# Performance work log

Measured on AMD Instinct MI355X. Metric: run time of the kernel, lower is better.

## Reference

```python
import jax, jax.numpy as jnp
import numpy as np
import math

B = 524288
D = 4
CTX = 64
HID = 128
IN_DIM = 2 + CTX  # keep_idx len is 2 for every mask
# default_masks_D(4, 10) dedups to exactly these 4 masks (torch module therefore has 4 layers)
KEEP = ((0, 1), (1, 2), (2, 3), (0, 3))
TRANS = ((2, 3), (0, 3), (0, 1), (1, 2))
L = 4


def _mlp(x, W1, b1, W2, b2, W3, b3):
    # MLP(in_dim, out_dim, hidden=128, depth=2): Lin+GELU, Lin+GELU, Lin
    x = jax.nn.gelu(x @ W1 + b1, approximate=False)
    x = jax.nn.gelu(x @ W2 + b2, approximate=False)
    return x @ W3 + b3


def setup_inputs() -> dict:
    key = jax.random.key(0)
    ks = jax.random.split(key, 16)
    theta = jax.random.normal(ks[0], (B, D), dtype=jnp.float32)
    h = jax.random.normal(ks[1], (B, CTX), dtype=jnp.float32)
    p = lambda k, shape: jax.random.normal(k, shape, dtype=jnp.float32) * 0.02
    inp = {"theta": theta, "h": h}
    # stacked per-layer weights for s_net and t_net
    for pref, off in (("s", 2), ("t", 8)):
        inp[pref + "W1"] = p(ks[off + 0], (L, IN_DIM, HID))
        inp[pref + "b1"] = p(ks[off + 1], (L, HID))
        inp[pref + "W2"] = p(ks[off + 2], (L, HID, HID))
        inp[pref + "b2"] = p(ks[off + 3], (L, HID))
        inp[pref + "W3"] = p(ks[off + 4], (L, HID, 2))
        inp[pref + "b3"] = p(ks[off + 5], (L, 2))
    return inp


def reference(theta, h, sW1, sb1, sW2, sb2, sW3, sb3, tW1, tb1, tW2, tb2, tW3, tb3):
    # ConditionalRealNVP.log_prob(theta, h)
    x = theta
    logdet = jnp.zeros(theta.shape[0], dtype=theta.dtype)
    for i in range(L):
        keep = np.array(KEEP[i])
        trans = np.array(TRANS[i])
        xp = jnp.concatenate([x[:, keep], h], axis=1)  # [B, 66]
        s = _mlp(xp, sW1[i], sb1[i], sW2[i], sb2[i], sW3[i], sb3[i])  # [B, 2]
        t = _mlp(xp, tW1[i], tb1[i], tW2[i], tb2[i], tW3[i], tb3[i])  # [B, 2]
        x = x.at[:, trans].set(x[:, trans] * jnp.exp(s) + t)
        logdet = logdet + s.sum(axis=1)
    log_pz = -0.5 * (x ** 2).sum(axis=1) - 0.5 * D * math.log(2 * math.pi)
    return log_pz + logdet
```

## Files before the change

### kernel.cpp

```cpp
#include <hip/hip_runtime.h>
#include <hip/hip_bf16.h>

typedef short short8 __attribute__((ext_vector_type(8)));
typedef float f32x4 __attribute__((ext_vector_type(4)));
typedef unsigned short u16;
typedef u16 u16x8 __attribute__((ext_vector_type(8)));

#define NL_STRIDE 57344
#define OFF_W1F 0
#define OFF_W2F 16384
#define OFF_W3F 49152
#define OFF_W1K 53248
#define OFF_B1  54272
#define OFF_B2  54784
#define OFF_B3  55296

__device__ __forceinline__ u16 f2bf(float f) {
  union { float f; unsigned int u; } v; v.f = f;
  unsigned int r = v.u + 0x7fffu + ((v.u >> 16) & 1u);
  return (u16)(r >> 16);
}

__device__ __forceinline__ float gelu_fast(float x) {
  float u = x * x;
  float t = fmaf(0.00417617f, u, -0.0560330f);
  t = fmaf(t, u, 0.394326f);
  float s = fmaf(x, t, 0.5f);
  s = __builtin_amdgcn_fmed3f(s, 0.0f, 1.0f);
  return x * s;
}

__global__ __launch_bounds__(256) void prep_kernel(
    const float* __restrict__ sW1, const float* __restrict__ sb1,
    const float* __restrict__ sW2, const float* __restrict__ sb2,
    const float* __restrict__ sW3, const float* __restrict__ sb3,
    const float* __restrict__ tW1, const float* __restrict__ tb1,
    const float* __restrict__ tW2, const float* __restrict__ tb2,
    const float* __restrict__ tW3, const float* __restrict__ tb3,
    char* __restrict__ ws)
{
  int nl = blockIdx.x;
  int layer = nl >> 1, net = nl & 1;
  const float* W1 = net ? tW1 : sW1;
  const float* W2 = net ? tW2 : sW2;
  const float* W3 = net ? tW3 : sW3;
  const float* B1 = net ? tb1 : sb1;
  const float* B2 = net ? tb2 : sb2;
  const float* B3 = net ? tb3 : sb3;
  char* base = ws + (size_t)nl * NL_STRIDE;
  int e = blockIdx.y * 256 + (int)threadIdx.x;

  if (e < 8192) {
    int kt = e >> 12, rem = e & 4095, nt = rem >> 9, r2 = rem & 511;
    int l = r2 >> 3, j = r2 & 7;
    int k = kt * 32 + (l >> 4) * 8 + j, n = nt * 16 + (l & 15);
    ((u16*)(base + OFF_W1F))[e] = f2bf(W1[layer * 8448 + (2 + k) * 128 + n]);
  } else if (e < 24576) {
    int e2 = e - 8192;
    int kt = e2 >> 12, nt = (e2 >> 9) & 7, l = (e2 >> 3) & 63, j = e2 & 7;
    int k = kt * 32 + (l >> 4) * 8 + j, n = nt * 16 + (l & 15);
    ((u16*)(base + OFF_W2F))[e2] = f2bf(W2[layer * 16384 + k * 128 + n]);
  } else if (e < 26624) {
    int e3 = e - 24576;
    int kt = e3 >> 9, l = (e3 >> 3) & 63, j = e3 & 7;
    int k = kt * 32 + (l >> 4) * 8 + j, n = l & 15;
    float v = (n < 2) ? W3[layer * 256 + k * 2 + n] : 0.0f;
    ((u16*)(base + OFF_W3F))[e3] = f2bf(v);
  } else if (e < 26880) {
    int e4 = e - 26624; int r = e4 >> 7, n = e4 & 127;
    ((float*)(base + OFF_W1K))[e4] = W1[layer * 8448 + r * 128 + n];
  } else if (e < 27008) {
    int e5 = e - 26880; ((float*)(base + OFF_B1))[e5] = B1[layer * 128 + e5];
  } else if (e < 27136) {
    int e6 = e - 27008; ((float*)(base + OFF_B2))[e6] = B2[layer * 128 + e6];
  } else if (e < 27138) {
    int e7 = e - 27136; ((float*)(base + OFF_B3))[e7] = B3[layer * 2 + e7];
  }
}

__global__ __launch_bounds__(256, 2) void realnvp_kernel(
    const float* __restrict__ theta, const float* __restrict__ h_g,
    const char* __restrict__ ws, float* __restrict__ out)
{
  __shared__ __align__(16) u16 hs[128 * 72];
  __shared__ __align__(16) u16 hid[128 * 136];
  __shared__ float x_lds[128 * 4];
  __shared__ float sbuf[2 * 128 * 2];

  const int tid = (int)threadIdx.x;
  const int row0 = (int)blockIdx.x * 128;
  const int wv = tid >> 6, lane = tid & 63, q = lane >> 4, lr = lane & 15;

  if (tid < 128) {
    float4 t4 = *(const float4*)(theta + (size_t)(row0 + tid) * 4);
    x_lds[tid * 4 + 0] = t4.x; x_lds[tid * 4 + 1] = t4.y;
    x_lds[tid * 4 + 2] = t4.z; x_lds[tid * 4 + 3] = t4.w;
  }
  {
    int r = tid >> 1, hf = tid & 1;
    const float* src = h_g + (size_t)(row0 + r) * 64 + hf * 32;
    u16* dst = &hs[r * 72 + hf * 32];
#pragma unroll
    for (int c = 0; c < 32; c += 8) {
      float4 f0 = *(const float4*)(src + c);
      float4 f1 = *(const float4*)(src + c + 4);
      u16x8 o;
      o[0] = f2bf(f0.x); o[1] = f2bf(f0.y); o[2] = f2bf(f0.z); o[3] = f2bf(f0.w);
      o[4] = f2bf(f1.x); o[5] = f2bf(f1.y); o[6] = f2bf(f1.z); o[7] = f2bf(f1.w);
      *(u16x8*)(dst + c) = o;
    }
  }
  __syncthreads();

  float logdet = 0.0f;
  const f32x4 zero4 = {0.f, 0.f, 0.f, 0.f};
  const int col0 = wv * 32 + lr;

#pragma unroll 1
  for (int layer = 0; layer < 4; ++layer) {
    int k0 = (0x0210 >> (layer * 4)) & 15;
    int k1 = (0x3321 >> (layer * 4)) & 15;

#pragma unroll 1
    for (int net = 0; net < 2; ++net) {
      const char* base = ws + (size_t)(layer * 2 + net) * NL_STRIDE;
      const u16* w1f = (const u16*)(base + OFF_W1F);
      const u16* w2f = (const u16*)(base + OFF_W2F);
      const u16* w3f = (const u16*)(base + OFF_W3F);
      const float* w1k = (const float*)(base + OFF_W1K);
      const float* b1 = (const float*)(base + OFF_B1);
      const float* b2 = (const float*)(base + OFF_B2);
      const float* b3 = (const float*)(base + OFF_B3);

      f32x4 acc[8][2];
#pragma unroll
      for (int mt = 0; mt < 8; ++mt) { acc[mt][0] = zero4; acc[mt][1] = zero4; }
      {
        const u16* abase = &hs[lr * 72 + q * 8];
#pragma unroll
        for (int kt = 0; kt < 2; ++kt) {
          short8 a[8];
#pragma unroll
          for (int mt = 0; mt < 8; ++mt)
            a[mt] = *(const short8*)(abase + mt * (16 * 72) + kt * 32);
          short8 b0 = *(const short8*)(w1f + (kt * 8 + wv * 2 + 0) * 512 + lane * 8);
          short8 b1v = *(const short8*)(w1f + (kt * 8 + wv * 2 + 1) * 512 + lane * 8);
#pragma unroll
          for (int mt = 0; mt < 8; ++mt) {
            acc[mt][0] = __builtin_amdgcn_mfma_f32_16x16x32_bf16(a[mt], b0, acc[mt][0], 0, 0, 0);
            acc[mt][1] = __builtin_amdgcn_mfma_f32_16x16x32_bf16(a[mt], b1v, acc[mt][1], 0, 0, 0);
          }
        }
      }
      float wk00 = w1k[col0],       wk01 = w1k[col0 + 16];
      float wk10 = w1k[128 + col0], wk11 = w1k[128 + col0 + 16];
      float bb0 = b1[col0], bb1 = b1[col0 + 16];
      __syncthreads();
#pragma unroll
      for (int mt = 0; mt < 8; ++mt) {
        int rb = mt * 16 + q * 4;
#pragma unroll
        for (int r = 0; r < 4; ++r) {
          int row = rb + r;
          float xk0 = x_lds[row * 4 + k0], xk1 = x_lds[row * 4 + k1];
          float v0 = acc[mt][0][r] + xk0 * wk00 + xk1 * wk10 + bb0;
          float v1 = acc[mt][1][r] + xk0 * wk01 + xk1 * wk11 + bb1;
          hid[row * 136 + col0]      = f2bf(gelu_fast(v0));
          hid[row * 136 + col0 + 16] = f2bf(gelu_fast(v1));
        }
      }
      __syncthreads();

      f32x4 acc2[8][2];
#pragma unroll
      for (int mt = 0; mt < 8; ++mt) { acc2[mt][0] = zero4; acc2[mt][1] = zero4; }
      {
        const u16* hbase = &hid[lr * 136 + q * 8];
#pragma unroll
        for (int kt = 0; kt < 4; ++kt) {
          short8 a[8];
#pragma unroll
          for (int mt = 0; mt < 8; ++mt)
            a[mt] = *(const short8*)(hbase + mt * (16 * 136) + kt * 32);
          short8 b0 = *(const short8*)(w2f + (kt * 8 + wv * 2 + 0) * 512 + lane * 8);
          short8 b1v = *(const short8*)(w2f + (kt * 8 + wv * 2 + 1) * 512 + lane * 8);
#pragma unroll
          for (int mt = 0; mt < 8; ++mt) {
            acc2[mt][0] = __builtin_amdgcn_mfma_f32_16x16x32_bf16(a[mt], b0, acc2[mt][0], 0, 0, 0);
            acc2[mt][1] = __builtin_amdgcn_mfma_f32_16x16x32_bf16(a[mt], b1v, acc2[mt][1], 0, 0, 0);
          }
        }
      }
      float cb0 = b2[col0], cb1 = b2[col0 + 16];
      __syncthreads();
#pragma unroll
      for (int mt = 0; mt < 8; ++mt) {
        int rb = mt * 16 + q * 4;
#pragma unroll
        for (int r = 0; r < 4; ++r) {
          int row = rb + r;
          hid[row * 136 + col0]      = f2bf(gelu_fast(acc2[mt][0][r] + cb0));
          hid[row * 136 + col0 + 16] = f2bf(gelu_fast(acc2[mt][1][r] + cb1));
        }
      }
      __syncthreads();

      f32x4 acc3[2]; acc3[0] = zero4; acc3[1] = zero4;
#pragma unroll
      for (int kt = 0; kt < 4; ++kt) {
        short8 b = *(const short8*)(w3f + kt * 512 + lane * 8);
#pragma unroll
        for (int i = 0; i < 2; ++i) {
          short8 a = *(const short8*)(&hid[((wv * 2 + i) * 16 + lr) * 136 + kt * 32 + q * 8]);
          acc3[i] = __builtin_amdgcn_mfma_f32_16x16x32_bf16(a, b, acc3[i], 0, 0, 0);
        }
      }
      if (lr < 2) {
        float bb = b3[lr];
#pragma unroll
        for (int i = 0; i < 2; ++i) {
          int rb = (wv * 2 + i) * 16 + q * 4;
#pragma unroll
          for (int r = 0; r < 4; ++r)
            sbuf[net * 256 + (rb + r) * 2 + lr] = acc3[i][r] + bb;
        }
      }
      __syncthreads();
    }

    if (tid < 128) {
      float s0 = sbuf[tid * 2 + 0], s1 = sbuf[tid * 2 + 1];
      float t0 = sbuf[256 + tid * 2 + 0], t1 = sbuf[256 + tid * 2 + 1];
      int a0 = (0x1002 >> (layer * 4)) & 15;
      int a1 = (0x2133 >> (layer * 4)) & 15;
      x_lds[tid * 4 + a0] = x_lds[tid * 4 + a0] * __expf(s0) + t0;
      x_lds[tid * 4 + a1] = x_lds[tid * 4 + a1] * __expf(s1) + t1;
      logdet += s0 + s1;
    }
    __syncthreads();
  }

  if (tid < 128) {
    float x0 = x_lds[tid * 4 + 0], x1 = x_lds[tid * 4 + 1];
    float x2 = x_lds[tid * 4 + 2], x3 = x_lds[tid * 4 + 3];
    out[row0 + tid] = -0.5f * (x0 * x0 + x1 * x1 + x2 * x2 + x3 * x3)
                      - 3.6757541328f + logdet;
  }
}

extern "C" void kernel_launch(void* const* d_in, const int* in_sizes, int n_in,
                              void* d_out, int out_size, void* d_ws, size_t ws_size,
                              hipStream_t stream) {
  (void)in_sizes; (void)n_in; (void)out_size; (void)ws_size;
  const float* theta = (const float*)d_in[0];
  const float* h     = (const float*)d_in[1];
  const float* sW1 = (const float*)d_in[2],  *sb1 = (const float*)d_in[3];
  const float* sW2 = (const float*)d_in[4],  *sb2 = (const float*)d_in[5];
  const float* sW3 = (const float*)d_in[6],  *sb3 = (const float*)d_in[7];
  const float* tW1 = (const float*)d_in[8],  *tb1 = (const float*)d_in[9];
  const float* tW2 = (const float*)d_in[10], *tb2 = (const float*)d_in[11];
  const float* tW3 = (const float*)d_in[12], *tb3 = (const float*)d_in[13];
  float* out = (float*)d_out;
  char* ws = (char*)d_ws;

  dim3 pgrid(8, 107);
  prep_kernel<<<pgrid, 256, 0, stream>>>(sW1, sb1, sW2, sb2, sW3, sb3,
                                         tW1, tb1, tW2, tb2, tW3, tb3, ws);
  realnvp_kernel<<<4096, 256, 0, stream>>>(theta, h, (const char*)ws, out);
}
```

Baseline: 615.0 us.

## Swizzle LDS layouts, pack bf16 conversions, permute hidden columns, raise occupancy to 3

Drops the padded LDS rows and uses XOR-swizzled addressing for the h and hidden tiles to avoid bank conflicts while shrinking shared memory. Hidden activations are stored as packed bf16 pairs through a column permutation, and the W2/W3 K-rows are permuted to match. Conversion uses the hardware v_cvt_pk_bf16_f32 instruction, GELU is evaluated on two values at once, and the per-layer keep inputs are staged in a compact xk buffer. Launch bounds rise to 3 blocks per CU, which tightens the register budget and risks spills.

```diff
diff --git a/kernel.cpp b/kernel.cpp
--- a/kernel.cpp
+++ b/kernel.cpp
@@ -3,8 +3,10 @@
 
 typedef short short8 __attribute__((ext_vector_type(8)));
 typedef float f32x4 __attribute__((ext_vector_type(4)));
+typedef float f32x2 __attribute__((ext_vector_type(2)));
 typedef unsigned short u16;
-typedef u16 u16x8 __attribute__((ext_vector_type(8)));
+typedef unsigned int u32;
+typedef u32 u32x4 __attribute__((ext_vector_type(4)));
 
 #define NL_STRIDE 57344
 #define OFF_W1F 0
@@ -21,13 +23,24 @@
   return (u16)(r >> 16);
 }
 
-__device__ __forceinline__ float gelu_fast(float x) {
-  float u = x * x;
-  float t = fmaf(0.00417617f, u, -0.0560330f);
-  t = fmaf(t, u, 0.394326f);
-  float s = fmaf(x, t, 0.5f);
-  s = __builtin_amdgcn_fmed3f(s, 0.0f, 1.0f);
+__device__ __forceinline__ u32 cvt_pk_bf16(float lo, float hi) {
+  u32 r;
+  asm("v_cvt_pk_bf16_f32 %0, %1, %2" : "=v"(r) : "v"(lo), "v"(hi));
+  return r;
+}
+
+__device__ __forceinline__ f32x2 gelu2(f32x2 x) {
+  f32x2 u = x * x;
+  f32x2 t = u * 0.00417617f + (-0.0560330f);
+  t = t * u + 0.394326f;
+  f32x2 s = x * t + 0.5f;
+  s.x = __builtin_amdgcn_fmed3f(s.x, 0.0f, 1.0f);
+  s.y = __builtin_amdgcn_fmed3f(s.y, 0.0f, 1.0f);
   return x * s;
+}
+
+__device__ __forceinline__ int perm_col(int p) {
+  return (p & ~31) | ((p & 1) << 4) | ((p & 31) >> 1);
 }
 
 __global__ __launch_bounds__(256) void prep_kernel(
@@ -58,13 +71,15 @@
   } else if (e < 24576) {
     int e2 = e - 8192;
     int kt = e2 >> 12, nt = (e2 >> 9) & 7, l = (e2 >> 3) & 63, j = e2 & 7;
-    int k = kt * 32 + (l >> 4) * 8 + j, n = nt * 16 + (l & 15);
-    ((u16*)(base + OFF_W2F))[e2] = f2bf(W2[layer * 16384 + k * 128 + n]);
+    int kp = kt * 32 + (l >> 4) * 8 + j, n = nt * 16 + (l & 15);
+    int c = perm_col(kp);
+    ((u16*)(base + OFF_W2F))[e2] = f2bf(W2[layer * 16384 + c * 128 + n]);
   } else if (e < 26624) {
     int e3 = e - 24576;
     int kt = e3 >> 9, l = (e3 >> 3) & 63, j = e3 & 7;
-    int k = kt * 32 + (l >> 4) * 8 + j, n = l & 15;
-    float v = (n < 2) ? W3[layer * 256 + k * 2 + n] : 0.0f;
+    int kp = kt * 32 + (l >> 4) * 8 + j, n = l & 15;
+    int c = perm_col(kp);
+    float v = (n < 2) ? W3[layer * 256 + c * 2 + n] : 0.0f;
     ((u16*)(base + OFF_W3F))[e3] = f2bf(v);
   } else if (e < 26880) {
     int e4 = e - 26624; int r = e4 >> 7, n = e4 & 127;
@@ -78,36 +93,43 @@
   }
 }
 
-__global__ __launch_bounds__(256, 2) void realnvp_kernel(
+__global__ __launch_bounds__(256, 3) void realnvp_kernel(
     const float* __restrict__ theta, const float* __restrict__ h_g,
     const char* __restrict__ ws, float* __restrict__ out)
 {
-  __shared__ __align__(16) u16 hs[128 * 72];
-  __shared__ __align__(16) u16 hid[128 * 136];
-  __shared__ float x_lds[128 * 4];
+  __shared__ __align__(16) u16 hs[128 * 64];
+  __shared__ __align__(16) u16 hid[128 * 128];
+  __shared__ __align__(16) float x_lds[128 * 4];
+  __shared__ __align__(8)  float xk_lds[128 * 2];
   __shared__ float sbuf[2 * 128 * 2];
 
   const int tid = (int)threadIdx.x;
   const int row0 = (int)blockIdx.x * 128;
   const int wv = tid >> 6, lane = tid & 63, q = lane >> 4, lr = lane & 15;
+  const char* hsB = (const char*)hs;
+  char* hidB = (char*)hid;
+  const int swz = (lr & 7) << 4;
 
   if (tid < 128) {
     float4 t4 = *(const float4*)(theta + (size_t)(row0 + tid) * 4);
-    x_lds[tid * 4 + 0] = t4.x; x_lds[tid * 4 + 1] = t4.y;
-    x_lds[tid * 4 + 2] = t4.z; x_lds[tid * 4 + 3] = t4.w;
+    *(f32x4*)&x_lds[tid * 4] = (f32x4){t4.x, t4.y, t4.z, t4.w};
+    xk_lds[tid * 2 + 0] = t4.x;
+    xk_lds[tid * 2 + 1] = t4.y;
   }
   {
     int r = tid >> 1, hf = tid & 1;
     const float* src = h_g + (size_t)(row0 + r) * 64 + hf * 32;
-    u16* dst = &hs[r * 72 + hf * 32];
+    const int wswz = (r & 7) << 4;
 #pragma unroll
     for (int c = 0; c < 32; c += 8) {
       float4 f0 = *(const float4*)(src + c);
       float4 f1 = *(const float4*)(src + c + 4);
-      u16x8 o;
-      o[0] = f2bf(f0.x); o[1] = f2bf(f0.y); o[2] = f2bf(f0.z); o[3] = f2bf(f0.w);
-      o[4] = f2bf(f1.x); o[5] = f2bf(f1.y); o[6] = f2bf(f1.z); o[7] = f2bf(f1.w);
-      *(u16x8*)(dst + c) = o;
+      u32x4 o;
+      o[0] = cvt_pk_bf16(f0.x, f0.y);
+      o[1] = cvt_pk_bf16(f0.z, f0.w);
+      o[2] = cvt_pk_bf16(f1.x, f1.y);
+      o[3] = cvt_pk_bf16(f1.z, f1.w);
+      *(u32x4*)((char*)hs + (((r * 64 + hf * 32 + c) * 2) ^ wswz)) = o;
     }
   }
   __syncthreads();
@@ -116,11 +138,15 @@
   const f32x4 zero4 = {0.f, 0.f, 0.f, 0.f};
   const int col0 = wv * 32 + lr;
 
+  unsigned wb[4];
+#pragma unroll
+  for (int r = 0; r < 4; ++r) {
+    int rl = q * 4 + r;
+    wb[r] = (unsigned)((rl * 256 + wv * 64 + lr * 4) ^ ((rl & 7) << 4));
+  }
+
 #pragma unroll 1
   for (int layer = 0; layer < 4; ++layer) {
-    int k0 = (0x0210 >> (layer * 4)) & 15;
-    int k1 = (0x3321 >> (layer * 4)) & 15;
-
 #pragma unroll 1
     for (int net = 0; net < 2; ++net) {
       const char* base = ws + (size_t)(layer * 2 + net) * NL_STRIDE;
@@ -135,38 +161,36 @@
       f32x4 acc[8][2];
 #pragma unroll
       for (int mt = 0; mt < 8; ++mt) { acc[mt][0] = zero4; acc[mt][1] = zero4; }
-      {
-        const u16* abase = &hs[lr * 72 + q * 8];
-#pragma unroll
-        for (int kt = 0; kt < 2; ++kt) {
-          short8 a[8];
-#pragma unroll
-          for (int mt = 0; mt < 8; ++mt)
-            a[mt] = *(const short8*)(abase + mt * (16 * 72) + kt * 32);
-          short8 b0 = *(const short8*)(w1f + (kt * 8 + wv * 2 + 0) * 512 + lane * 8);
-          short8 b1v = *(const short8*)(w1f + (kt * 8 + wv * 2 + 1) * 512 + lane * 8);
-#pragma unroll
-          for (int mt = 0; mt < 8; ++mt) {
-            acc[mt][0] = __builtin_amdgcn_mfma_f32_16x16x32_bf16(a[mt], b0, acc[mt][0], 0, 0, 0);
-            acc[mt][1] = __builtin_amdgcn_mfma_f32_16x16x32_bf16(a[mt], b1v, acc[mt][1], 0, 0, 0);
-          }
-        }
-      }
-      float wk00 = w1k[col0],       wk01 = w1k[col0 + 16];
-      float wk10 = w1k[128 + col0], wk11 = w1k[128 + col0 + 16];
-      float bb0 = b1[col0], bb1 = b1[col0 + 16];
+#pragma unroll
+      for (int kt = 0; kt < 2; ++kt) {
+        const int abase = (((lr * 64 + kt * 32 + q * 8) * 2)) ^ swz;
+        short8 a[8];
+#pragma unroll
+        for (int mt = 0; mt < 8; ++mt)
+          a[mt] = *(const short8*)(hsB + abase + mt * 2048);
+        short8 b0 = *(const short8*)(w1f + (kt * 8 + wv * 2 + 0) * 512 + lane * 8);
+        short8 b1v = *(const short8*)(w1f + (kt * 8 + wv * 2 + 1) * 512 + lane * 8);
+#pragma unroll
+        for (int mt = 0; mt < 8; ++mt) {
+          acc[mt][0] = __builtin_amdgcn_mfma_f32_16x16x32_bf16(a[mt], b0, acc[mt][0], 0, 0, 0);
+          acc[mt][1] = __builtin_amdgcn_mfma_f32_16x16x32_bf16(a[mt], b1v, acc[mt][1], 0, 0, 0);
+        }
+      }
+      f32x2 wk0 = {w1k[col0],       w1k[col0 + 16]};
+      f32x2 wk1 = {w1k[128 + col0], w1k[128 + col0 + 16]};
+      f32x2 bb  = {b1[col0],        b1[col0 + 16]};
       __syncthreads();
 #pragma unroll
       for (int mt = 0; mt < 8; ++mt) {
-        int rb = mt * 16 + q * 4;
 #pragma unroll
         for (int r = 0; r < 4; ++r) {
-          int row = rb + r;
-          float xk0 = x_lds[row * 4 + k0], xk1 = x_lds[row * 4 + k1];
-          float v0 = acc[mt][0][r] + xk0 * wk00 + xk1 * wk10 + bb0;
-          float v1 = acc[mt][1][r] + xk0 * wk01 + xk1 * wk11 + bb1;
-          hid[row * 136 + col0]      = f2bf(gelu_fast(v0));
-          hid[row * 136 + col0 + 16] = f2bf(gelu_fast(v1));
+          int row = mt * 16 + q * 4 + r;
+          f32x2 xk = *(const f32x2*)(xk_lds + row * 2);
+          f32x2 v = (f32x2){acc[mt][0][r], acc[mt][1][r]} + bb;
+          v = xk.x * wk0 + v;
+          v = xk.y * wk1 + v;
+          f32x2 g = gelu2(v);
+          *(u32*)(hidB + (wb[r] + mt * 4096)) = cvt_pk_bf16(g.x, g.y);
         }
       }
       __syncthreads();
@@ -174,33 +198,30 @@
       f32x4 acc2[8][2];
 #pragma unroll
       for (int mt = 0; mt < 8; ++mt) { acc2[mt][0] = zero4; acc2[mt][1] = zero4; }
-      {
-        const u16* hbase = &hid[lr * 136 + q * 8];
-#pragma unroll
-        for (int kt = 0; kt < 4; ++kt) {
-          short8 a[8];
-#pragma unroll
-          for (int mt = 0; mt < 8; ++mt)
-            a[mt] = *(const short8*)(hbase + mt * (16 * 136) + kt * 32);
-          short8 b0 = *(const short8*)(w2f + (kt * 8 + wv * 2 + 0) * 512 + lane * 8);
-          short8 b1v = *(const short8*)(w2f + (kt * 8 + wv * 2 + 1) * 512 + lane * 8);
-#pragma unroll
-          for (int mt = 0; mt < 8; ++mt) {
-            acc2[mt][0] = __builtin_amdgcn_mfma_f32_16x16x32_bf16(a[mt], b0, acc2[mt][0], 0, 0, 0);
-            acc2[mt][1] = __builtin_amdgcn_mfma_f32_16x16x32_bf16(a[mt], b1v, acc2[mt][1], 0, 0, 0);
-          }
-        }
-      }
-      float cb0 = b2[col0], cb1 = b2[col0 + 16];
+#pragma unroll
+      for (int kt = 0; kt < 4; ++kt) {
+        const int abase = ((lr * 256 + kt * 64 + q * 16)) ^ swz;
+        short8 a[8];
+#pragma unroll
+        for (int mt = 0; mt < 8; ++mt)
+          a[mt] = *(const short8*)(hidB + abase + mt * 4096);
+        short8 b0 = *(const short8*)(w2f + (kt * 8 + wv * 2 + 0) * 512 + lane * 8);
+        short8 b1v = *(const short8*)(w2f + (kt * 8 + wv * 2 + 1) * 512 + lane * 8);
+#pragma unroll
+        for (int mt = 0; mt < 8; ++mt) {
+          acc2[mt][0] = __builtin_amdgcn_mfma_f32_16x16x32_bf16(a[mt], b0, acc2[mt][0], 0, 0, 0);
+          acc2[mt][1] = __builtin_amdgcn_mfma_f32_16x16x32_bf16(a[mt], b1v, acc2[mt][1], 0, 0, 0);
+        }
+      }
+      f32x2 cbb = {b2[col0], b2[col0 + 16]};
       __syncthreads();
 #pragma unroll
       for (int mt = 0; mt < 8; ++mt) {
-        int rb = mt * 16 + q * 4;
 #pragma unroll
         for (int r = 0; r < 4; ++r) {
-          int row = rb + r;
-          hid[row * 136 + col0]      = f2bf(gelu_fast(acc2[mt][0][r] + cb0));
-          hid[row * 136 + col0 + 16] = f2bf(gelu_fast(acc2[mt][1][r] + cb1));
+          f32x2 v = (f32x2){acc2[mt][0][r], acc2[mt][1][r]} + cbb;
+          f32x2 g = gelu2(v);
+          *(u32*)(hidB + (wb[r] + mt * 4096)) = cvt_pk_bf16(g.x, g.y);
         }
       }
       __syncthreads();
@@ -209,20 +230,21 @@
 #pragma unroll
       for (int kt = 0; kt < 4; ++kt) {
         short8 b = *(const short8*)(w3f + kt * 512 + lane * 8);
+        const int abase = ((lr * 256 + kt * 64 + q * 16)) ^ swz;
 #pragma unroll
         for (int i = 0; i < 2; ++i) {
-          short8 a = *(const short8*)(&hid[((wv * 2 + i) * 16 + lr) * 136 + kt * 32 + q * 8]);
+          short8 a = *(const short8*)(hidB + abase + (wv * 2 + i) * 4096);
           acc3[i] = __builtin_amdgcn_mfma_f32_16x16x32_bf16(a, b, acc3[i], 0, 0, 0);
         }
       }
       if (lr < 2) {
-        float bb = b3[lr];
+        float bbv = b3[lr];
 #pragma unroll
         for (int i = 0; i < 2; ++i) {
           int rb = (wv * 2 + i) * 16 + q * 4;
 #pragma unroll
           for (int r = 0; r < 4; ++r)
-            sbuf[net * 256 + (rb + r) * 2 + lr] = acc3[i][r] + bb;
+            sbuf[net * 256 + (rb + r) * 2 + lr] = acc3[i][r] + bbv;
         }
       }
       __syncthreads();
@@ -236,6 +258,11 @@
       x_lds[tid * 4 + a0] = x_lds[tid * 4 + a0] * __expf(s0) + t0;
       x_lds[tid * 4 + a1] = x_lds[tid * 4 + a1] * __expf(s1) + t1;
       logdet += s0 + s1;
+      int nl_ = (layer + 1) & 3;
+      int nk0 = (0x0210 >> (nl_ * 4)) & 15;
+      int nk1 = (0x3321 >> (nl_ * 4)) & 15;
+      xk_lds[tid * 2 + 0] = x_lds[tid * 4 + nk0];
+      xk_lds[tid * 2 + 1] = x_lds[tid * 4 + nk1];
     }
     __syncthreads();
   }
```

Result: faster. 582.2 us (-5.3%).
